# Kernel optimization log

Measured on AMD Instinct MI355X. Metric: run time of the kernel, lower is better.

## Reference

```python
import jax, jax.numpy as jnp
import numpy as np

EPS = 1e-8  # masked_log_softmax default eps


def setup_inputs() -> dict:
    key = jax.random.key(0)
    k1, k2, k3, k4, k5, k6 = jax.random.split(key, 6)
    B, T, S, L, D = 8, 128, 256, 256, 512  # batch, tgt_len, src_len(enc), src_length(proj), d_model
    decoder_hidden_state = jax.random.normal(k1, (B, T, D), dtype=jnp.float32)
    encoder_outputs = jax.random.normal(k2, (B, S, D), dtype=jnp.float32)
    mask = (jax.random.uniform(k3, (B, T, S)) > 0.3).astype(jnp.float32)
    W1 = jax.random.normal(k4, (L, D), dtype=jnp.float32) * 0.02  # Linear(d_model, src_length).weight
    W2 = jax.random.normal(k5, (L, D), dtype=jnp.float32) * 0.02
    vt = jax.random.normal(k6, (L,), dtype=jnp.float32) * 0.02   # Linear(src_length, 1).weight
    return {"decoder_hidden_state": decoder_hidden_state, "encoder_outputs": encoder_outputs,
            "mask": mask, "W1": W1, "W2": W2, "vt": vt}


def reference(decoder_hidden_state, encoder_outputs, mask, W1, W2, vt):
    # decoder_transform: (B, T, 1, L); encoder_transform: (B, 1, S, L)
    dec_t = jnp.einsum('btd,ld->btl', decoder_hidden_state, W1)[:, :, None, :]
    enc_t = jnp.einsum('bsd,ld->bsl', encoder_outputs, W2)[:, None, :, :]
    weights = jnp.tanh(dec_t + enc_t)                     # (B, T, S, L)
    scores = jnp.einsum('btsl,l->bts', weights, vt)       # vt reduction, squeeze(-1)
    logits = scores + jnp.log(mask + EPS)                 # masked log-softmax over src
    return jax.nn.log_softmax(logits, axis=-1)
```

## Files before the change

kernel.cpp:

```cpp
#include <hip/hip_runtime.h>

typedef __attribute__((ext_vector_type(8))) short short8;
typedef __attribute__((ext_vector_type(4))) float f32x4;

#define TANH_SCALE 2.8853900817779268f
#define LOG_EPS   -18.420680743952367f

static __device__ __forceinline__ unsigned short f2bf(float f) {
  unsigned u = __builtin_bit_cast(unsigned, f);
  u += 0x7FFFu + ((u >> 16) & 1u);
  return (unsigned short)(u >> 16);
}
static __device__ __forceinline__ float bf2f(unsigned short h) {
  unsigned u = (unsigned)h << 16;
  return __builtin_bit_cast(float, u);
}

__global__ __launch_bounds__(256) void cvt_all(
    const float4* __restrict__ dec, const float4* __restrict__ enc,
    const float4* __restrict__ W1, const float4* __restrict__ W2,
    ushort4* __restrict__ dec_b, ushort4* __restrict__ enc_b,
    ushort4* __restrict__ w1_b, ushort4* __restrict__ w2_b) {
  int i = blockIdx.x * 256 + threadIdx.x;
  const float4* src; ushort4* dst; int off;
  if (i < 131072)            { src = dec; dst = dec_b; off = 0; }
  else if (i < 131072+262144){ src = enc; dst = enc_b; off = 131072; }
  else if (i < 131072+262144+32768) { src = W1; dst = w1_b; off = 131072+262144; }
  else                       { src = W2; dst = w2_b; off = 131072+262144+32768; }
  int j = i - off;
  float4 v = src[j];
  ushort4 o;
  o.x = f2bf(v.x); o.y = f2bf(v.y); o.z = f2bf(v.z); o.w = f2bf(v.w);
  dst[j] = o;
}

__global__ __launch_bounds__(256) void gemm_proj(
    const unsigned short* __restrict__ w1b, const unsigned short* __restrict__ w2b,
    const unsigned short* __restrict__ decb, const unsigned short* __restrict__ encb,
    float* __restrict__ decPt, unsigned short* __restrict__ encPb) {
  const int K = 512;
  int idx = blockIdx.x;
  const unsigned short *A, *Bp;
  int N, mt, nt;
  bool is_dec = (idx < 128);
  size_t cbase;
  if (is_dec) {
    A = w1b; Bp = decb; N = 1024;
    mt = idx >> 5; nt = idx & 31;
    cbase = 0;
  } else {
    int j = idx - 128, z = j >> 5, rem = j & 31;
    A = w2b; Bp = encb + (size_t)z * 256 * K; N = 256;
    mt = rem >> 3; nt = rem & 7;
    cbase = (size_t)z * 256 * 256;
  }
  const int tid = threadIdx.x, wave = tid >> 6, lane = tid & 63;
  const int m0 = mt * 64 + wave * 16;
  const int n0 = nt * 32;
  const int l16 = lane & 15, quad = lane >> 4, kb = quad * 8;

  f32x4 acc0 = {0.f,0.f,0.f,0.f}, acc1 = {0.f,0.f,0.f,0.f};

  const unsigned short* ap  = A + (long)(m0 + l16) * K + kb;
  const unsigned short* bp0 = Bp + (long)(n0 + l16) * K + kb;

  for (int ks = 0; ks < K; ks += 32) {
    short8 a  = *(const short8*)(ap + ks);
    short8 b0 = *(const short8*)(bp0 + ks);
    short8 b1 = *(const short8*)(bp0 + 16 * K + ks);
    acc0 = __builtin_amdgcn_mfma_f32_16x16x32_bf16(a, b0, acc0, 0, 0, 0);
    acc1 = __builtin_amdgcn_mfma_f32_16x16x32_bf16(a, b1, acc1, 0, 0, 0);
  }

  f32x4 accs[2] = {acc0, acc1};
  if (is_dec) {
#pragma unroll
    for (int j = 0; j < 2; ++j) {
      int n = n0 + j * 16 + l16;
#pragma unroll
      for (int r = 0; r < 4; ++r) {
        int m = m0 + quad * 4 + r;
        decPt[(long)m * N + n] = __builtin_amdgcn_exp2f(accs[j][r] * TANH_SCALE);
      }
    }
  } else {
#pragma unroll
    for (int j = 0; j < 2; ++j) {
      int n = n0 + j * 16 + l16;
#pragma unroll
      for (int r = 0; r < 4; ++r) {
        int m = m0 + quad * 4 + r;
        encPb[cbase + (long)m * N + n] =
            f2bf(__builtin_amdgcn_exp2f(accs[j][r] * TANH_SCALE));
      }
    }
  }
}

__global__ __launch_bounds__(1024) void fused_score_softmax(
    const float* __restrict__ decPt, const unsigned short* __restrict__ encPb,
    const float* __restrict__ mask, const float* __restrict__ vt,
    float* __restrict__ out) {
  const int T = 128, S = 256, L = 256;
  const int b = blockIdx.x >> 5;
  const int t0 = (blockIdx.x & 31) * 4;
  const int s = threadIdx.x & 255;
  const int q = threadIdx.x >> 8;
  const int l0 = q * (L / 4);

  const unsigned short* __restrict__ ep = encPb + (size_t)b * L * S + (size_t)l0 * S + s;
  const float* __restrict__ dp = decPt + (size_t)(b * T + t0) + (size_t)l0 * 1024;

  float acc0 = 0.f, acc1 = 0.f, acc2 = 0.f, acc3 = 0.f;
#pragma unroll 8
  for (int l = 0; l < L / 4; ++l) {
    float e = bf2f(ep[(size_t)l * S]);
    float4 P = *(const float4*)(dp + (size_t)l * 1024);
    float v = vt[l0 + l];
    float r0 = __builtin_amdgcn_rcpf(fmaf(P.x, e, 1.0f));
    float r1 = __builtin_amdgcn_rcpf(fmaf(P.y, e, 1.0f));
    float r2 = __builtin_amdgcn_rcpf(fmaf(P.z, e, 1.0f));
    float r3 = __builtin_amdgcn_rcpf(fmaf(P.w, e, 1.0f));
    acc0 = fmaf(v, r0, acc0);
    acc1 = fmaf(v, r1, acc1);
    acc2 = fmaf(v, r2, acc2);
    acc3 = fmaf(v, r3, acc3);
  }

  __shared__ float partial[4][4][256];
  partial[q][0][s] = acc0;
  partial[q][1][s] = acc1;
  partial[q][2][s] = acc2;
  partial[q][3][s] = acc3;
  __syncthreads();

  float lg = partial[0][q][s] + partial[1][q][s] + partial[2][q][s] + partial[3][q][s];

  const float LN2 = 0.6931471805599453f, L2E = 1.4426950408889634f;
  {
    float m = mask[(size_t)(b * T + t0 + q) * S + s];
    lg = fmaf(-2.0f, lg, (m != 0.0f) ? 0.0f : LOG_EPS);
  }

  __shared__ float redm[16], reds[16];
  const int wid = threadIdx.x >> 6, lane = threadIdx.x & 63;

  float w = lg;
#pragma unroll
  for (int off = 1; off < 64; off <<= 1) w = fmaxf(w, __shfl_xor(w, off));
  if (lane == 0) redm[wid] = w;
  __syncthreads();
  float bm = fmaxf(fmaxf(redm[q * 4 + 0], redm[q * 4 + 1]),
                   fmaxf(redm[q * 4 + 2], redm[q * 4 + 3]));

  float e = __builtin_amdgcn_exp2f((lg - bm) * L2E);
#pragma unroll
  for (int off = 1; off < 64; off <<= 1) e += __shfl_xor(e, off);
  if (lane == 0) reds[wid] = e;
  __syncthreads();
  float sum = reds[q * 4 + 0] + reds[q * 4 + 1] + reds[q * 4 + 2] + reds[q * 4 + 3];

  out[(size_t)(b * T + t0 + q) * S + s] = lg - bm - LN2 * __builtin_amdgcn_logf(sum);
}

extern "C" void kernel_launch(void* const* d_in, const int* in_sizes, int n_in,
                              void* d_out, int out_size, void* d_ws, size_t ws_size,
                              hipStream_t stream) {
  const int B = 8, T = 128, S = 256, L = 256, D = 512;
  const float* dec = (const float*)d_in[0];
  const float* enc = (const float*)d_in[1];
  const float* mask = (const float*)d_in[2];
  const float* W1 = (const float*)d_in[3];
  const float* W2 = (const float*)d_in[4];
  const float* vt = (const float*)d_in[5];
  float* out = (float*)d_out;

  char* ws = (char*)d_ws;
  unsigned short* dec_b = (unsigned short*)(ws);
  unsigned short* enc_b = (unsigned short*)(ws + (1u << 20));
  unsigned short* w1_b  = (unsigned short*)(ws + 3u * (1u << 20));
  unsigned short* w2_b  = (unsigned short*)(ws + 3u * (1u << 20) + (256u << 10));
  float* decPt = (float*)(ws + 3u * (1u << 20) + (512u << 10));
  unsigned short* encPb = (unsigned short*)(ws + 4u * (1u << 20) + (512u << 10));

  cvt_all<<<1792, 256, 0, stream>>>(
      (const float4*)dec, (const float4*)enc, (const float4*)W1, (const float4*)W2,
      (ushort4*)dec_b, (ushort4*)enc_b, (ushort4*)w1_b, (ushort4*)w2_b);

  gemm_proj<<<384, 256, 0, stream>>>(w1_b, w2_b, dec_b, enc_b, decPt, encPb);

  fused_score_softmax<<<B * T / 4, 1024, 0, stream>>>(decPt, encPb, mask, vt, out);
  (void)in_sizes; (void)n_in; (void)out_size; (void)ws_size; (void)D;
}
```

Measured before the change: 97.39 us.

## Merge three kernels into one cooperative kernel with grid-wide syncs

```diff
diff --git a/kernel.cpp b/kernel.cpp
--- a/kernel.cpp
+++ b/kernel.cpp
@@ -1,4 +1,7 @@
 #include <hip/hip_runtime.h>
+#include <hip/hip_cooperative_groups.h>
+
+namespace cg = cooperative_groups;
 
 typedef __attribute__((ext_vector_type(8))) short short8;
 typedef __attribute__((ext_vector_type(4))) float f32x4;
@@ -16,157 +19,154 @@
   return __builtin_bit_cast(float, u);
 }
 
-__global__ __launch_bounds__(256) void cvt_all(
+__global__ __launch_bounds__(1024) void ptr_attn_all(
     const float4* __restrict__ dec, const float4* __restrict__ enc,
+    const float* __restrict__ mask,
     const float4* __restrict__ W1, const float4* __restrict__ W2,
-    ushort4* __restrict__ dec_b, ushort4* __restrict__ enc_b,
-    ushort4* __restrict__ w1_b, ushort4* __restrict__ w2_b) {
-  int i = blockIdx.x * 256 + threadIdx.x;
-  const float4* src; ushort4* dst; int off;
-  if (i < 131072)            { src = dec; dst = dec_b; off = 0; }
-  else if (i < 131072+262144){ src = enc; dst = enc_b; off = 131072; }
-  else if (i < 131072+262144+32768) { src = W1; dst = w1_b; off = 131072+262144; }
-  else                       { src = W2; dst = w2_b; off = 131072+262144+32768; }
-  int j = i - off;
-  float4 v = src[j];
-  ushort4 o;
-  o.x = f2bf(v.x); o.y = f2bf(v.y); o.z = f2bf(v.z); o.w = f2bf(v.w);
-  dst[j] = o;
-}
+    const float* __restrict__ vt,
+    unsigned short* __restrict__ dec_b, unsigned short* __restrict__ enc_b,
+    unsigned short* __restrict__ w1_b, unsigned short* __restrict__ w2_b,
+    float* __restrict__ decPt, unsigned short* __restrict__ encPb,
+    float* __restrict__ out) {
+  cg::grid_group grid = cg::this_grid();
+  const int tid = threadIdx.x;
 
-__global__ __launch_bounds__(256) void gemm_proj(
-    const unsigned short* __restrict__ w1b, const unsigned short* __restrict__ w2b,
-    const unsigned short* __restrict__ decb, const unsigned short* __restrict__ encb,
-    float* __restrict__ decPt, unsigned short* __restrict__ encPb) {
-  const int K = 512;
-  int idx = blockIdx.x;
-  const unsigned short *A, *Bp;
-  int N, mt, nt;
-  bool is_dec = (idx < 128);
-  size_t cbase;
-  if (is_dec) {
-    A = w1b; Bp = decb; N = 1024;
-    mt = idx >> 5; nt = idx & 31;
-    cbase = 0;
-  } else {
-    int j = idx - 128, z = j >> 5, rem = j & 31;
-    A = w2b; Bp = encb + (size_t)z * 256 * K; N = 256;
-    mt = rem >> 3; nt = rem & 7;
-    cbase = (size_t)z * 256 * 256;
+  {
+    int idx = blockIdx.x * 1024 + tid;
+    for (int j = idx; j < 458752; j += 262144) {
+      const float4* src; ushort4* dst; int off;
+      if (j < 131072)            { src = dec; dst = (ushort4*)dec_b; off = 0; }
+      else if (j < 393216)       { src = enc; dst = (ushort4*)enc_b; off = 131072; }
+      else if (j < 425984)       { src = W1;  dst = (ushort4*)w1_b;  off = 393216; }
+      else                       { src = W2;  dst = (ushort4*)w2_b;  off = 425984; }
+      int k = j - off;
+      float4 v = src[k];
+      ushort4 o;
+      o.x = f2bf(v.x); o.y = f2bf(v.y); o.z = f2bf(v.z); o.w = f2bf(v.w);
+      dst[k] = o;
+    }
   }
-  const int tid = threadIdx.x, wave = tid >> 6, lane = tid & 63;
-  const int m0 = mt * 64 + wave * 16;
-  const int n0 = nt * 32;
-  const int l16 = lane & 15, quad = lane >> 4, kb = quad * 8;
+  grid.sync();
 
-  f32x4 acc0 = {0.f,0.f,0.f,0.f}, acc1 = {0.f,0.f,0.f,0.f};
+  {
+    const int q = tid >> 8;
+    const int sub = q * 256 + blockIdx.x;
+    if (sub < 768) {
+      const int K = 512;
+      const unsigned short *A, *Bp;
+      int N, mt, nt;
+      bool is_dec = (sub < 256);
+      size_t cbase = 0;
+      if (is_dec) {
+        A = w1_b; Bp = dec_b; N = 1024;
+        mt = sub >> 6; nt = sub & 63;
+      } else {
+        int e = sub - 256, z = e >> 6, rem = e & 63;
+        A = w2_b; Bp = enc_b + (size_t)z * 256 * K; N = 256;
+        mt = rem >> 4; nt = rem & 15;
+        cbase = (size_t)z * 256 * 256;
+      }
+      const int st = tid & 255;
+      const int wave = st >> 6, lane = st & 63;
+      const int m0 = mt * 64 + wave * 16;
+      const int n0 = nt * 16;
+      const int l16 = lane & 15, quad = lane >> 4, kb = quad * 8;
 
-  const unsigned short* ap  = A + (long)(m0 + l16) * K + kb;
-  const unsigned short* bp0 = Bp + (long)(n0 + l16) * K + kb;
-
-  for (int ks = 0; ks < K; ks += 32) {
-    short8 a  = *(const short8*)(ap + ks);
-    short8 b0 = *(const short8*)(bp0 + ks);
-    short8 b1 = *(const short8*)(bp0 + 16 * K + ks);
-    acc0 = __builtin_amdgcn_mfma_f32_16x16x32_bf16(a, b0, acc0, 0, 0, 0);
-    acc1 = __builtin_amdgcn_mfma_f32_16x16x32_bf16(a, b1, acc1, 0, 0, 0);
-  }
-
-  f32x4 accs[2] = {acc0, acc1};
-  if (is_dec) {
+      f32x4 acc = {0.f, 0.f, 0.f, 0.f};
+      const unsigned short* ap = A + (long)(m0 + l16) * K + kb;
+      const unsigned short* bp = Bp + (long)(n0 + l16) * K + kb;
+#pragma unroll 4
+      for (int ks = 0; ks < K; ks += 32) {
+        short8 a = *(const short8*)(ap + ks);
+        short8 b = *(const short8*)(bp + ks);
+        acc = __builtin_amdgcn_mfma_f32_16x16x32_bf16(a, b, acc, 0, 0, 0);
+      }
+      int n = n0 + l16;
+      if (is_dec) {
 #pragma unroll
-    for (int j = 0; j < 2; ++j) {
-      int n = n0 + j * 16 + l16;
+        for (int r = 0; r < 4; ++r) {
+          int m = m0 + quad * 4 + r;
+          decPt[(long)m * N + n] = __builtin_amdgcn_exp2f(acc[r] * TANH_SCALE);
+        }
+      } else {
 #pragma unroll
-      for (int r = 0; r < 4; ++r) {
-        int m = m0 + quad * 4 + r;
-        decPt[(long)m * N + n] = __builtin_amdgcn_exp2f(accs[j][r] * TANH_SCALE);
-      }
-    }
-  } else {
-#pragma unroll
-    for (int j = 0; j < 2; ++j) {
-      int n = n0 + j * 16 + l16;
-#pragma unroll
-      for (int r = 0; r < 4; ++r) {
-        int m = m0 + quad * 4 + r;
-        encPb[cbase + (long)m * N + n] =
-            f2bf(__builtin_amdgcn_exp2f(accs[j][r] * TANH_SCALE));
+        for (int r = 0; r < 4; ++r) {
+          int m = m0 + quad * 4 + r;
+          encPb[cbase + (long)m * N + n] =
+              f2bf(__builtin_amdgcn_exp2f(acc[r] * TANH_SCALE));
+        }
       }
     }
   }
-}
+  grid.sync();
 
-__global__ __launch_bounds__(1024) void fused_score_softmax(
-    const float* __restrict__ decPt, const unsigned short* __restrict__ encPb,
-    const float* __restrict__ mask, const float* __restrict__ vt,
-    float* __restrict__ out) {
-  const int T = 128, S = 256, L = 256;
-  const int b = blockIdx.x >> 5;
-  const int t0 = (blockIdx.x & 31) * 4;
-  const int s = threadIdx.x & 255;
-  const int q = threadIdx.x >> 8;
-  const int l0 = q * (L / 4);
+  {
+    const int T = 128, S = 256, L = 256;
+    const int b = blockIdx.x >> 5;
+    const int t0 = (blockIdx.x & 31) * 4;
+    const int s = tid & 255;
+    const int q = tid >> 8;
+    const int l0 = q * (L / 4);
 
-  const unsigned short* __restrict__ ep = encPb + (size_t)b * L * S + (size_t)l0 * S + s;
-  const float* __restrict__ dp = decPt + (size_t)(b * T + t0) + (size_t)l0 * 1024;
+    const unsigned short* __restrict__ ep = encPb + (size_t)b * L * S + (size_t)l0 * S + s;
+    const float* __restrict__ dp = decPt + (size_t)(b * T + t0) + (size_t)l0 * 1024;
 
-  float acc0 = 0.f, acc1 = 0.f, acc2 = 0.f, acc3 = 0.f;
+    float acc0 = 0.f, acc1 = 0.f, acc2 = 0.f, acc3 = 0.f;
 #pragma unroll 8
-  for (int l = 0; l < L / 4; ++l) {
-    float e = bf2f(ep[(size_t)l * S]);
-    float4 P = *(const float4*)(dp + (size_t)l * 1024);
-    float v = vt[l0 + l];
-    float r0 = __builtin_amdgcn_rcpf(fmaf(P.x, e, 1.0f));
-    float r1 = __builtin_amdgcn_rcpf(fmaf(P.y, e, 1.0f));
-    float r2 = __builtin_amdgcn_rcpf(fmaf(P.z, e, 1.0f));
-    float r3 = __builtin_amdgcn_rcpf(fmaf(P.w, e, 1.0f));
-    acc0 = fmaf(v, r0, acc0);
-    acc1 = fmaf(v, r1, acc1);
-    acc2 = fmaf(v, r2, acc2);
-    acc3 = fmaf(v, r3, acc3);
+    for (int l = 0; l < L / 4; ++l) {
+      float e = bf2f(ep[(size_t)l * S]);
+      float4 P = *(const float4*)(dp + (size_t)l * 1024);
+      float v = vt[l0 + l];
+      float r0 = __builtin_amdgcn_rcpf(fmaf(P.x, e, 1.0f));
+      float r1 = __builtin_amdgcn_rcpf(fmaf(P.y, e, 1.0f));
+      float r2 = __builtin_amdgcn_rcpf(fmaf(P.z, e, 1.0f));
+      float r3 = __builtin_amdgcn_rcpf(fmaf(P.w, e, 1.0f));
+      acc0 = fmaf(v, r0, acc0);
+      acc1 = fmaf(v, r1, acc1);
+      acc2 = fmaf(v, r2, acc2);
+      acc3 = fmaf(v, r3, acc3);
+    }
+
+    __shared__ float partial[4][4][256];
+    partial[q][0][s] = acc0;
+    partial[q][1][s] = acc1;
+    partial[q][2][s] = acc2;
+    partial[q][3][s] = acc3;
+    __syncthreads();
+
+    float lg = partial[0][q][s] + partial[1][q][s] + partial[2][q][s] + partial[3][q][s];
+
+    const float LN2 = 0.6931471805599453f, L2E = 1.4426950408889634f;
+    {
+      float m = mask[(size_t)(b * T + t0 + q) * S + s];
+      lg = fmaf(-2.0f, lg, (m != 0.0f) ? 0.0f : LOG_EPS);
+    }
+
+    __shared__ float redm[16], reds[16];
+    const int wid = tid >> 6, lane = tid & 63;
+
+    float w = lg;
+#pragma unroll
+    for (int off = 1; off < 64; off <<= 1) w = fmaxf(w, __shfl_xor(w, off));
+    if (lane == 0) redm[wid] = w;
+    __syncthreads();
+    float bm = fmaxf(fmaxf(redm[q * 4 + 0], redm[q * 4 + 1]),
+                     fmaxf(redm[q * 4 + 2], redm[q * 4 + 3]));
+
+    float e = __builtin_amdgcn_exp2f((lg - bm) * L2E);
+#pragma unroll
+    for (int off = 1; off < 64; off <<= 1) e += __shfl_xor(e, off);
+    if (lane == 0) reds[wid] = e;
+    __syncthreads();
+    float sum = reds[q * 4 + 0] + reds[q * 4 + 1] + reds[q * 4 + 2] + reds[q * 4 + 3];
+
+    out[(size_t)(b * T + t0 + q) * S + s] = lg - bm - LN2 * __builtin_amdgcn_logf(sum);
   }
-
-  __shared__ float partial[4][4][256];
-  partial[q][0][s] = acc0;
-  partial[q][1][s] = acc1;
-  partial[q][2][s] = acc2;
-  partial[q][3][s] = acc3;
-  __syncthreads();
-
-  float lg = partial[0][q][s] + partial[1][q][s] + partial[2][q][s] + partial[3][q][s];
-
-  const float LN2 = 0.6931471805599453f, L2E = 1.4426950408889634f;
-  {
-    float m = mask[(size_t)(b * T + t0 + q) * S + s];
-    lg = fmaf(-2.0f, lg, (m != 0.0f) ? 0.0f : LOG_EPS);
-  }
-
-  __shared__ float redm[16], reds[16];
-  const int wid = threadIdx.x >> 6, lane = threadIdx.x & 63;
-
-  float w = lg;
-#pragma unroll
-  for (int off = 1; off < 64; off <<= 1) w = fmaxf(w, __shfl_xor(w, off));
-  if (lane == 0) redm[wid] = w;
-  __syncthreads();
-  float bm = fmaxf(fmaxf(redm[q * 4 + 0], redm[q * 4 + 1]),
-                   fmaxf(redm[q * 4 + 2], redm[q * 4 + 3]));
-
-  float e = __builtin_amdgcn_exp2f((lg - bm) * L2E);
-#pragma unroll
-  for (int off = 1; off < 64; off <<= 1) e += __shfl_xor(e, off);
-  if (lane == 0) reds[wid] = e;
-  __syncthreads();
-  float sum = reds[q * 4 + 0] + reds[q * 4 + 1] + reds[q * 4 + 2] + reds[q * 4 + 3];
-
-  out[(size_t)(b * T + t0 + q) * S + s] = lg - bm - LN2 * __builtin_amdgcn_logf(sum);
 }
 
 extern "C" void kernel_launch(void* const* d_in, const int* in_sizes, int n_in,
                               void* d_out, int out_size, void* d_ws, size_t ws_size,
                               hipStream_t stream) {
-  const int B = 8, T = 128, S = 256, L = 256, D = 512;
   const float* dec = (const float*)d_in[0];
   const float* enc = (const float*)d_in[1];
   const float* mask = (const float*)d_in[2];
@@ -183,12 +183,11 @@
   float* decPt = (float*)(ws + 3u * (1u << 20) + (512u << 10));
   unsigned short* encPb = (unsigned short*)(ws + 4u * (1u << 20) + (512u << 10));
 
-  cvt_all<<<1792, 256, 0, stream>>>(
-      (const float4*)dec, (const float4*)enc, (const float4*)W1, (const float4*)W2,
-      (ushort4*)dec_b, (ushort4*)enc_b, (ushort4*)w1_b, (ushort4*)w2_b);
-
-  gemm_proj<<<384, 256, 0, stream>>>(w1_b, w2_b, dec_b, enc_b, decPt, encPb);
-
-  fused_score_softmax<<<B * T / 4, 1024, 0, stream>>>(decPt, encPb, mask, vt, out);
-  (void)in_sizes; (void)n_in; (void)out_size; (void)ws_size; (void)D;
+  void* args[] = {
+      (void*)&dec, (void*)&enc, (void*)&mask, (void*)&W1, (void*)&W2, (void*)&vt,
+      (void*)&dec_b, (void*)&enc_b, (void*)&w1_b, (void*)&w2_b,
+      (void*)&decPt, (void*)&encPb, (void*)&out};
+  hipLaunchCooperativeKernel((const void*)ptr_attn_all, dim3(256), dim3(1024),
+                             args, 0, stream);
+  (void)in_sizes; (void)n_in; (void)out_size; (void)ws_size;
 }
```

New measurement: 174.6 us. 1.79x slower.
